# Optimization experiments

Hardware: AMD Instinct MI355X
Metric: run time of the kernel (lower is better)

The kernel has to match this reference:

```python
import jax, jax.numpy as jnp
import numpy as np

B, I, O, K = 4096, 1024, 1024, 16

def setup_inputs() -> dict:
    key = jax.random.key(0)
    k1, k2 = jax.random.split(key)
    x = jax.random.normal(k1, (B, I), dtype=jnp.float32)
    weights = jax.random.normal(k2, (O, I, K), dtype=jnp.float32)
    bias = jnp.zeros((O,), dtype=jnp.float32)
    centers = jnp.linspace(-1.0, 1.0, K, dtype=jnp.float32)
    widths = jnp.full((K,), 0.1, dtype=jnp.float32)
    return {"x": x, "weights": weights, "bias": bias, "centers": centers, "widths": widths}

def reference(x, weights, bias, centers, widths):
    # Gaussian RBF basis: [B, I, K]
    diff = x[:, :, None] - centers[None, None, :]
    kernels = jnp.exp(-(diff ** 2) / (2.0 * widths[None, None, :] ** 2))
    # Contraction over input_dim and num_kernels (GEMM-equivalent)
    out = jnp.einsum('bik,oik->bo', kernels, weights)
    return out + bias
```

## Files before the change

kernel.cpp:

```cpp
#include <hip/hip_runtime.h>
#include <hip/hip_bf16.h>


#define B_DIM 4096
#define I_DIM 1024
#define O_DIM 1024
#define NK 16
#define KD (I_DIM * NK)

typedef unsigned short u16;
typedef __attribute__((ext_vector_type(8))) __bf16 bf16x8;
typedef __attribute__((ext_vector_type(4))) float f32x4;
typedef __attribute__((ext_vector_type(8))) unsigned short u16x8;

typedef const __attribute__((address_space(1))) unsigned short gu16;
typedef __attribute__((address_space(3))) unsigned short lu16;

static __device__ __forceinline__ u16 f2bf(float f) {
  unsigned u = __float_as_uint(f);
  u += 0x7FFFu + ((u >> 16) & 1u);
  return (u16)(u >> 16);
}

__global__ void __launch_bounds__(256) rbf_feat(const float* __restrict__ x,
                                                u16* __restrict__ feat,
                                                const float* __restrict__ centers,
                                                const float* __restrict__ widths) {
  const int idx = blockIdx.x * 256 + threadIdx.x;
  const float xv = x[idx];
  u16x8 lo, hi;
#pragma unroll
  for (int k = 0; k < 16; ++k) {
    const float c = centers[k];
    const float w = widths[k];
    const float s = -0.5f * __builtin_amdgcn_rcpf(w * w);
    const float d = xv - c;
    const u16 h = f2bf(__expf(d * d * s));
    if (k < 8) lo[k] = h; else hi[k - 8] = h;
  }
  u16x8* dst = (u16x8*)(feat + (size_t)idx * 16);
  dst[0] = lo;
  dst[1] = hi;
}

__global__ void __launch_bounds__(256) cvt_w(const float4* __restrict__ w,
                                             u16x8* __restrict__ wb) {
  const size_t i = (size_t)blockIdx.x * 256 + threadIdx.x;
  const float4 a = w[2 * i];
  const float4 b = w[2 * i + 1];
  u16x8 o;
  o[0] = f2bf(a.x); o[1] = f2bf(a.y); o[2] = f2bf(a.z); o[3] = f2bf(a.w);
  o[4] = f2bf(b.x); o[5] = f2bf(b.y); o[6] = f2bf(b.z); o[7] = f2bf(b.w);
  wb[i] = o;
}

static __device__ __forceinline__ void stage_half(const u16* __restrict__ g,
                                                  u16* __restrict__ lds, int t) {
#pragma unroll
  for (int j = 0; j < 2; ++j) {
    const int chunk = j * 512 + t;
    const int row = chunk >> 3, slot = chunk & 7;
    const int c = slot ^ (row & 7);
    __builtin_amdgcn_global_load_lds((gu16*)(g + (size_t)row * KD + c * 8),
                                     (lu16*)(lds + chunk * 8), 16, 0, 0);
  }
}

#define NT 64

__global__ void __launch_bounds__(512, 2)
gemm8(const u16* __restrict__ A, const u16* __restrict__ Bm,
      float* __restrict__ part) {
  __shared__ u16 sA[2][2][128 * 64];
  __shared__ u16 sB[2][2][128 * 64];

  const int t = threadIdx.x;
  const int bm = blockIdx.x;
  const int bn = blockIdx.y;
  const int kz = blockIdx.z;
  const int wid = t >> 6, l = t & 63;
  const int wr = wid >> 2, wc = wid & 3;
  const int lm = l & 15, lk = l >> 4;

  const u16* aT = A + (size_t)(bm * 256) * KD + kz * 4096;
  const u16* bT = Bm + (size_t)(bn * 256) * KD + kz * 4096;

  const int swz0 = ((0 * 4 + lk) ^ (lm & 7)) * 8;
  const int swz1 = ((1 * 4 + lk) ^ (lm & 7)) * 8;
  const int arow = wr * 64 + lm;
  const int brow = wc * 32 + lm;

  f32x4 acc[8][4];
#pragma unroll
  for (int i = 0; i < 8; ++i)
#pragma unroll
    for (int j = 0; j < 4; ++j)
      acc[i][j] = (f32x4){0.f, 0.f, 0.f, 0.f};

  bf16x8 aq[4][2];
  bf16x8 b0[2][2];
  bf16x8 b1[2][2];

  stage_half(aT, &sA[0][0][0], t);
  stage_half(aT + (size_t)128 * KD, &sA[0][1][0], t);
  stage_half(bT, &sB[0][0][0], t);
  stage_half(bT + (size_t)128 * KD, &sB[0][1][0], t);
  stage_half(bT + 64, &sB[1][0][0], t);
  stage_half(aT + 64, &sA[1][0][0], t);
  asm volatile("s_waitcnt vmcnt(4)" ::: "memory");
  __builtin_amdgcn_s_barrier();

  for (int T = 0; T < NT; ++T) {
    const int c = T & 1;

#pragma unroll
    for (int mi = 0; mi < 4; ++mi) {
      aq[mi][0] = *(const bf16x8*)&sA[c][0][(arow + mi * 16) * 64 + swz0];
      aq[mi][1] = *(const bf16x8*)&sA[c][0][(arow + mi * 16) * 64 + swz1];
    }
#pragma unroll
    for (int ni = 0; ni < 2; ++ni) {
      b0[ni][0] = *(const bf16x8*)&sB[c][0][(brow + ni * 16) * 64 + swz0];
      b0[ni][1] = *(const bf16x8*)&sB[c][0][(brow + ni * 16) * 64 + swz1];
    }
    if (T + 1 < NT)
      stage_half(aT + (size_t)128 * KD + (T + 1) * 64, &sA[(T + 1) & 1][1][0], t);
    __builtin_amdgcn_s_barrier();
    asm volatile("s_waitcnt lgkmcnt(0)" ::: "memory");
    __builtin_amdgcn_sched_barrier(0);
    __builtin_amdgcn_s_setprio(1);
#pragma unroll
    for (int mi = 0; mi < 4; ++mi)
#pragma unroll
      for (int ni = 0; ni < 2; ++ni)
#pragma unroll
        for (int kk = 0; kk < 2; ++kk)
          acc[mi][ni] = __builtin_amdgcn_mfma_f32_16x16x32_bf16(
              aq[mi][kk], b0[ni][kk], acc[mi][ni], 0, 0, 0);
    __builtin_amdgcn_s_setprio(0);
    __builtin_amdgcn_s_barrier();

#pragma unroll
    for (int ni = 0; ni < 2; ++ni) {
      b1[ni][0] = *(const bf16x8*)&sB[c][1][(brow + ni * 16) * 64 + swz0];
      b1[ni][1] = *(const bf16x8*)&sB[c][1][(brow + ni * 16) * 64 + swz1];
    }
    if (T + 1 < NT)
      stage_half(bT + (size_t)128 * KD + (T + 1) * 64, &sB[(T + 1) & 1][1][0], t);
    __builtin_amdgcn_s_barrier();
    asm volatile("s_waitcnt lgkmcnt(0)" ::: "memory");
    __builtin_amdgcn_sched_barrier(0);
    __builtin_amdgcn_s_setprio(1);
#pragma unroll
    for (int mi = 0; mi < 4; ++mi)
#pragma unroll
      for (int ni = 0; ni < 2; ++ni)
#pragma unroll
        for (int kk = 0; kk < 2; ++kk)
          acc[mi][2 + ni] = __builtin_amdgcn_mfma_f32_16x16x32_bf16(
              aq[mi][kk], b1[ni][kk], acc[mi][2 + ni], 0, 0, 0);
    __builtin_amdgcn_s_setprio(0);
    __builtin_amdgcn_s_barrier();

#pragma unroll
    for (int mi = 0; mi < 4; ++mi) {
      aq[mi][0] = *(const bf16x8*)&sA[c][1][(arow + mi * 16) * 64 + swz0];
      aq[mi][1] = *(const bf16x8*)&sA[c][1][(arow + mi * 16) * 64 + swz1];
    }
    if (T + 2 < NT)
      stage_half(bT + (T + 2) * 64, &sB[T & 1][0][0], t);
    __builtin_amdgcn_s_barrier();
    asm volatile("s_waitcnt lgkmcnt(0)" ::: "memory");
    __builtin_amdgcn_sched_barrier(0);
    __builtin_amdgcn_s_setprio(1);
#pragma unroll
    for (int mi = 0; mi < 4; ++mi)
#pragma unroll
      for (int ni = 0; ni < 2; ++ni)
#pragma unroll
        for (int kk = 0; kk < 2; ++kk)
          acc[4 + mi][2 + ni] = __builtin_amdgcn_mfma_f32_16x16x32_bf16(
              aq[mi][kk], b1[ni][kk], acc[4 + mi][2 + ni], 0, 0, 0);
    __builtin_amdgcn_s_setprio(0);
    __builtin_amdgcn_s_barrier();

    if (T + 2 < NT)
      stage_half(aT + (T + 2) * 64, &sA[T & 1][0][0], t);
    __builtin_amdgcn_s_barrier();
    asm volatile("s_waitcnt lgkmcnt(0)" ::: "memory");
    __builtin_amdgcn_sched_barrier(0);
    __builtin_amdgcn_s_setprio(1);
#pragma unroll
    for (int mi = 0; mi < 4; ++mi)
#pragma unroll
      for (int ni = 0; ni < 2; ++ni)
#pragma unroll
        for (int kk = 0; kk < 2; ++kk)
          acc[4 + mi][ni] = __builtin_amdgcn_mfma_f32_16x16x32_bf16(
              aq[mi][kk], b0[ni][kk], acc[4 + mi][ni], 0, 0, 0);
    __builtin_amdgcn_s_setprio(0);
    if (T + 2 < NT) asm volatile("s_waitcnt vmcnt(4)" ::: "memory");
    else            asm volatile("s_waitcnt vmcnt(0)" ::: "memory");
    __builtin_amdgcn_s_barrier();
  }

  float* pW = part + (size_t)kz * ((size_t)B_DIM * O_DIM);
#pragma unroll
  for (int qa = 0; qa < 2; ++qa)
#pragma unroll
    for (int mi = 0; mi < 4; ++mi)
#pragma unroll
      for (int qb = 0; qb < 2; ++qb)
#pragma unroll
        for (int ni = 0; ni < 2; ++ni) {
          const int row0 = bm * 256 + qa * 128 + wr * 64 + mi * 16 + lk * 4;
          const int col = bn * 256 + qb * 128 + wc * 32 + ni * 16 + lm;
#pragma unroll
          for (int j = 0; j < 4; ++j)
            pW[(size_t)(row0 + j) * O_DIM + col] = acc[qa * 4 + mi][qb * 2 + ni][j];
        }
}

__global__ void __launch_bounds__(256) reduce4(const float4* __restrict__ p,
                                               const float4* __restrict__ bias4,
                                               float4* __restrict__ out) {
  const int i = blockIdx.x * 256 + threadIdx.x;
  const size_t s = (size_t)B_DIM * O_DIM / 4;
  const float4 a = p[i], b = p[i + s], c = p[i + 2 * s], d = p[i + 3 * s];
  const float4 bb = bias4[i & 255];
  float4 r;
  r.x = a.x + b.x + c.x + d.x + bb.x;
  r.y = a.y + b.y + c.y + d.y + bb.y;
  r.z = a.z + b.z + c.z + d.z + bb.z;
  r.w = a.w + b.w + c.w + d.w + bb.w;
  out[i] = r;
}

#define BM 128
#define BN 64
#define BK 64

__global__ void __launch_bounds__(256, 2) gemm_bt(const u16* __restrict__ A,
                                                  const u16* __restrict__ Bm,
                                                  const float* __restrict__ bias,
                                                  float* __restrict__ C) {
  __shared__ u16 sA[BM * BK];
  __shared__ u16 sB[BN * BK];

  const int t = threadIdx.x;
  const int bm = blockIdx.x, bn = blockIdx.y;
  const int wid = t >> 6, l = t & 63;
  const int wr = wid >> 1, wc = wid & 1;
  const int lm = l & 15, lk = l >> 4;

  const u16* aG = A + (size_t)bm * BM * KD;
  const u16* bG = Bm + (size_t)bn * BN * KD;

  f32x4 acc[4][2];
#pragma unroll
  for (int mi = 0; mi < 4; ++mi)
#pragma unroll
    for (int ni = 0; ni < 2; ++ni)
      acc[mi][ni] = (f32x4){0.f, 0.f, 0.f, 0.f};

  for (int kt = 0; kt < KD; kt += BK) {
#pragma unroll
    for (int j = 0; j < 4; ++j) {
      const int chunk = j * 256 + t;
      const int row = chunk >> 3, slot = chunk & 7;
      const int c = slot ^ (row & 7);
      __builtin_amdgcn_global_load_lds((gu16*)(aG + (size_t)row * KD + kt + c * 8),
                                       (lu16*)(sA + chunk * 8), 16, 0, 0);
    }
#pragma unroll
    for (int j = 0; j < 2; ++j) {
      const int chunk = j * 256 + t;
      const int row = chunk >> 3, slot = chunk & 7;
      const int c = slot ^ (row & 7);
      __builtin_amdgcn_global_load_lds((gu16*)(bG + (size_t)row * KD + kt + c * 8),
                                       (lu16*)(sB + chunk * 8), 16, 0, 0);
    }
    __syncthreads();
#pragma unroll
    for (int kk = 0; kk < 2; ++kk) {
      const int s = (kk * 4 + lk) ^ (lm & 7);
      bf16x8 af[4], bfr[2];
#pragma unroll
      for (int mi = 0; mi < 4; ++mi)
        af[mi] = *(const bf16x8*)(sA + (wr * 64 + mi * 16 + lm) * BK + s * 8);
#pragma unroll
      for (int ni = 0; ni < 2; ++ni)
        bfr[ni] = *(const bf16x8*)(sB + (wc * 32 + ni * 16 + lm) * BK + s * 8);
#pragma unroll
      for (int mi = 0; mi < 4; ++mi)
#pragma unroll
        for (int ni = 0; ni < 2; ++ni)
          acc[mi][ni] = __builtin_amdgcn_mfma_f32_16x16x32_bf16(af[mi], bfr[ni],
                                                                acc[mi][ni], 0, 0, 0);
    }
    __syncthreads();
  }

#pragma unroll
  for (int ni = 0; ni < 2; ++ni) {
    const int col = bn * BN + wc * 32 + ni * 16 + lm;
    const float bv = bias[col];
#pragma unroll
    for (int mi = 0; mi < 4; ++mi) {
      const int row0 = bm * BM + wr * 64 + mi * 16 + lk * 4;
#pragma unroll
      for (int j = 0; j < 4; ++j)
        C[(size_t)(row0 + j) * O_DIM + col] = acc[mi][ni][j] + bv;
    }
  }
}

extern "C" void kernel_launch(void* const* d_in, const int* in_sizes, int n_in,
                              void* d_out, int out_size, void* d_ws, size_t ws_size,
                              hipStream_t stream) {
  const float* x = (const float*)d_in[0];
  const float* w = (const float*)d_in[1];
  const float* bias = (const float*)d_in[2];
  const float* centers = (const float*)d_in[3];
  const float* widths = (const float*)d_in[4];
  float* out = (float*)d_out;

  u16* feat = (u16*)d_ws;
  u16* wb = (u16*)((char*)d_ws + (size_t)B_DIM * KD * 2);
  float* part = (float*)((char*)d_ws + (size_t)B_DIM * KD * 2 + (size_t)O_DIM * KD * 2);

  rbf_feat<<<(B_DIM * I_DIM) / 256, 256, 0, stream>>>(x, feat, centers, widths);
  cvt_w<<<(O_DIM * KD) / (256 * 8), 256, 0, stream>>>((const float4*)w, (u16x8*)wb);

  const size_t need = (size_t)B_DIM * KD * 2 + (size_t)O_DIM * KD * 2 +
                      4ull * B_DIM * O_DIM * 4;
  if (ws_size >= need) {
    dim3 grid(B_DIM / 256, O_DIM / 256, 4);
    gemm8<<<grid, 512, 0, stream>>>(feat, wb, part);
    reduce4<<<(B_DIM * O_DIM / 4) / 256, 256, 0, stream>>>(
        (const float4*)part, (const float4*)bias, (float4*)out);
  } else {
    dim3 grid(B_DIM / BM, O_DIM / BN);
    gemm_bt<<<grid, 256, 0, stream>>>(feat, wb, bias, out);
  }
}
```

Baseline: 184.7 us.

## Merge four MFMA phases into two per iteration with fewer barriers

Restructures the main K loop from four load/compute phases into two. The first phase loads A half 0 plus both B halves and issues both next-tile half-1 global stages. The second phase loads A half 1 and issues both T+2 half-0 stages, cutting workgroup barriers and lgkmcnt waits per iteration. This relies on the compiler's own LDS waits and holds more fragments in registers at once, which risks higher VGPR pressure and less overlap granularity.

```diff
diff --git a/kernel.cpp b/kernel.cpp
--- a/kernel.cpp
+++ b/kernel.cpp
@@ -97,10 +97,6 @@
     for (int j = 0; j < 4; ++j)
       acc[i][j] = (f32x4){0.f, 0.f, 0.f, 0.f};
 
-  bf16x8 aq[4][2];
-  bf16x8 b0[2][2];
-  bf16x8 b1[2][2];
-
   stage_half(aT, &sA[0][0][0], t);
   stage_half(aT + (size_t)128 * KD, &sA[0][1][0], t);
   stage_half(bT, &sB[0][0][0], t);
@@ -113,6 +109,7 @@
   for (int T = 0; T < NT; ++T) {
     const int c = T & 1;
 
+    bf16x8 aq[4][2], b0[2][2], b1[2][2];
 #pragma unroll
     for (int mi = 0; mi < 4; ++mi) {
       aq[mi][0] = *(const bf16x8*)&sA[c][0][(arow + mi * 16) * 64 + swz0];
@@ -122,12 +119,14 @@
     for (int ni = 0; ni < 2; ++ni) {
       b0[ni][0] = *(const bf16x8*)&sB[c][0][(brow + ni * 16) * 64 + swz0];
       b0[ni][1] = *(const bf16x8*)&sB[c][0][(brow + ni * 16) * 64 + swz1];
-    }
-    if (T + 1 < NT)
+      b1[ni][0] = *(const bf16x8*)&sB[c][1][(brow + ni * 16) * 64 + swz0];
+      b1[ni][1] = *(const bf16x8*)&sB[c][1][(brow + ni * 16) * 64 + swz1];
+    }
+    if (T + 1 < NT) {
       stage_half(aT + (size_t)128 * KD + (T + 1) * 64, &sA[(T + 1) & 1][1][0], t);
-    __builtin_amdgcn_s_barrier();
-    asm volatile("s_waitcnt lgkmcnt(0)" ::: "memory");
-    __builtin_amdgcn_sched_barrier(0);
+      stage_half(bT + (size_t)128 * KD + (T + 1) * 64, &sB[(T + 1) & 1][1][0], t);
+    }
+
     __builtin_amdgcn_s_setprio(1);
 #pragma unroll
     for (int mi = 0; mi < 4; ++mi)
@@ -137,20 +136,6 @@
         for (int kk = 0; kk < 2; ++kk)
           acc[mi][ni] = __builtin_amdgcn_mfma_f32_16x16x32_bf16(
               aq[mi][kk], b0[ni][kk], acc[mi][ni], 0, 0, 0);
-    __builtin_amdgcn_s_setprio(0);
-    __builtin_amdgcn_s_barrier();
-
-#pragma unroll
-    for (int ni = 0; ni < 2; ++ni) {
-      b1[ni][0] = *(const bf16x8*)&sB[c][1][(brow + ni * 16) * 64 + swz0];
-      b1[ni][1] = *(const bf16x8*)&sB[c][1][(brow + ni * 16) * 64 + swz1];
-    }
-    if (T + 1 < NT)
-      stage_half(bT + (size_t)128 * KD + (T + 1) * 64, &sB[(T + 1) & 1][1][0], t);
-    __builtin_amdgcn_s_barrier();
-    asm volatile("s_waitcnt lgkmcnt(0)" ::: "memory");
-    __builtin_amdgcn_sched_barrier(0);
-    __builtin_amdgcn_s_setprio(1);
 #pragma unroll
     for (int mi = 0; mi < 4; ++mi)
 #pragma unroll
@@ -160,18 +145,22 @@
           acc[mi][2 + ni] = __builtin_amdgcn_mfma_f32_16x16x32_bf16(
               aq[mi][kk], b1[ni][kk], acc[mi][2 + ni], 0, 0, 0);
     __builtin_amdgcn_s_setprio(0);
-    __builtin_amdgcn_s_barrier();
-
-#pragma unroll
-    for (int mi = 0; mi < 4; ++mi) {
-      aq[mi][0] = *(const bf16x8*)&sA[c][1][(arow + mi * 16) * 64 + swz0];
-      aq[mi][1] = *(const bf16x8*)&sA[c][1][(arow + mi * 16) * 64 + swz1];
-    }
-    if (T + 2 < NT)
-      stage_half(bT + (T + 2) * 64, &sB[T & 1][0][0], t);
-    __builtin_amdgcn_s_barrier();
+
     asm volatile("s_waitcnt lgkmcnt(0)" ::: "memory");
     __builtin_amdgcn_sched_barrier(0);
+    __builtin_amdgcn_s_barrier();
+
+    bf16x8 aq2[4][2];
+#pragma unroll
+    for (int mi = 0; mi < 4; ++mi) {
+      aq2[mi][0] = *(const bf16x8*)&sA[c][1][(arow + mi * 16) * 64 + swz0];
+      aq2[mi][1] = *(const bf16x8*)&sA[c][1][(arow + mi * 16) * 64 + swz1];
+    }
+    if (T + 2 < NT) {
+      stage_half(bT + (T + 2) * 64, &sB[T & 1][0][0], t);
+      stage_half(aT + (T + 2) * 64, &sA[T & 1][0][0], t);
+    }
+
     __builtin_amdgcn_s_setprio(1);
 #pragma unroll
     for (int mi = 0; mi < 4; ++mi)
@@ -180,16 +169,7 @@
 #pragma unroll
         for (int kk = 0; kk < 2; ++kk)
           acc[4 + mi][2 + ni] = __builtin_amdgcn_mfma_f32_16x16x32_bf16(
-              aq[mi][kk], b1[ni][kk], acc[4 + mi][2 + ni], 0, 0, 0);
-    __builtin_amdgcn_s_setprio(0);
-    __builtin_amdgcn_s_barrier();
-
-    if (T + 2 < NT)
-      stage_half(aT + (T + 2) * 64, &sA[T & 1][0][0], t);
-    __builtin_amdgcn_s_barrier();
-    asm volatile("s_waitcnt lgkmcnt(0)" ::: "memory");
-    __builtin_amdgcn_sched_barrier(0);
-    __builtin_amdgcn_s_setprio(1);
+              aq2[mi][kk], b1[ni][kk], acc[4 + mi][2 + ni], 0, 0, 0);
 #pragma unroll
     for (int mi = 0; mi < 4; ++mi)
 #pragma unroll
@@ -197,8 +177,9 @@
 #pragma unroll
         for (int kk = 0; kk < 2; ++kk)
           acc[4 + mi][ni] = __builtin_amdgcn_mfma_f32_16x16x32_bf16(
-              aq[mi][kk], b0[ni][kk], acc[4 + mi][ni], 0, 0, 0);
+              aq2[mi][kk], b0[ni][kk], acc[4 + mi][ni], 0, 0, 0);
     __builtin_amdgcn_s_setprio(0);
+
     if (T + 2 < NT) asm volatile("s_waitcnt vmcnt(4)" ::: "memory");
     else            asm volatile("s_waitcnt vmcnt(0)" ::: "memory");
     __builtin_amdgcn_s_barrier();
```

Result: no change. 182.1 us (-1.4%).
